# Performance work log

Hardware: AMD Instinct MI355X
Metric: run time of the kernel (lower is better)

The kernel has to match this reference:

```python
import jax, jax.numpy as jnp
import numpy as np


def setup_inputs() -> dict:
    key = jax.random.key(0)
    ks = jax.random.split(key, 6)
    B, T, D, H = 2, 2048, 1024, 16
    dk = D // H
    s = 0.02
    return {
        "x": jax.random.normal(ks[0], (B, T, D), dtype=jnp.float32),
        "Wq": jax.random.normal(ks[1], (H, dk, dk), dtype=jnp.float32) * s,
        "Wk": jax.random.normal(ks[2], (H, dk, dk), dtype=jnp.float32) * s,
        "Wv": jax.random.normal(ks[3], (H, dk, dk), dtype=jnp.float32) * s,
        "Wp": jax.random.normal(ks[4], (D, D), dtype=jnp.float32) * s,
        "bp": jnp.zeros((D,), dtype=jnp.float32),
    }


def reference(x, Wq, Wk, Wv, Wp, bp):
    B, T, D = x.shape
    H, dk, _ = Wq.shape
    # split into heads: [B, H, T, dk]
    xh = x.reshape(B, T, H, dk).transpose(0, 2, 1, 3)
    # per-head torch Linear (y = x @ W^T), all heads at once
    q = jnp.einsum('bhtd,hkd->bhtk', xh, Wq)
    k = jnp.einsum('bhtd,hkd->bhtk', xh, Wk)
    v = jnp.einsum('bhtd,hkd->bhtk', xh, Wv)
    scale = 1.0 / jnp.sqrt(jnp.float32(dk))  # original divides by sqrt(C) with C == d_k
    scores = jnp.einsum('bhqd,bhkd->bhqk', q, k) * scale
    causal = jnp.tril(jnp.ones((T, T), dtype=bool))
    scores = jnp.where(causal[None, None], scores, -jnp.inf)
    attn = jax.nn.softmax(scores, axis=-1)
    out = jnp.einsum('bhqk,bhkd->bhqd', attn, v)  # [B,H,T,dk]
    out = out.transpose(0, 2, 1, 3).reshape(B, T, D)  # concat heads
    return out @ Wp.T + bp
```

## Files before the change

kernel.cpp:

```cpp
#include <hip/hip_runtime.h>
#include <math.h>

#define B_ 2
#define T_ 2048
#define D_ 1024
#define H_ 16
#define DK 64
#define BH_ (B_*H_)

typedef __attribute__((ext_vector_type(8))) short short8;
typedef __attribute__((ext_vector_type(4))) float fragC;

#define MFMA32(A,B,C) __builtin_amdgcn_mfma_f32_16x16x32_bf16((A),(B),(C),0,0,0)

__device__ __forceinline__ unsigned short f2bf(float x) {
    union { float f; unsigned u; } c; c.f = x;
    unsigned r = c.u + 0x7fff + ((c.u >> 16) & 1);
    return (unsigned short)(r >> 16);
}

__device__ __forceinline__ unsigned pack2bf(float a, float b) {
    return (unsigned)f2bf(a) | ((unsigned)f2bf(b) << 16);
}

__device__ __forceinline__ unsigned permpack(float a, float b) {
    union { float f; unsigned u; } ca, cb; ca.f = a; cb.f = b;
    return __builtin_amdgcn_perm(cb.u, ca.u, 0x07060302);
}

__device__ __forceinline__ short8 packbf8(float4 a, float4 b) {
    union { short8 v; unsigned u[4]; } r;
    r.u[0] = pack2bf(a.x, a.y); r.u[1] = pack2bf(a.z, a.w);
    r.u[2] = pack2bf(b.x, b.y); r.u[3] = pack2bf(b.z, b.w);
    return r.v;
}

__device__ __forceinline__ void gload_lds16(const void* g, void* l) {
    __builtin_amdgcn_global_load_lds(
        (const __attribute__((address_space(1))) unsigned int*)g,
        (__attribute__((address_space(3))) unsigned int*)l, 16, 0, 0);
}

__global__ __launch_bounds__(256) void qkv_kernel(
    const float* __restrict__ x,
    const float* __restrict__ Wq, const float* __restrict__ Wk,
    const float* __restrict__ Wv, const float* __restrict__ Wp,
    unsigned short* __restrict__ Wb,
    unsigned short* __restrict__ q, unsigned short* __restrict__ k,
    unsigned short* __restrict__ vt)
{
    __shared__ unsigned short Wl[3*64*64];

    const int bh = blockIdx.x;
    const int b  = bh >> 4, h = bh & 15;
    const int t0 = blockIdx.y * 128;
    const int tid = threadIdx.x;
    const int wave = tid >> 6, lane = tid & 63;
    const int n = lane & 15, quad = lane >> 4;

    {
        const int L = bh + (blockIdx.y << 5);
        const float* src = Wp + (size_t)L*2048 + tid*8;
        float4 a = *(const float4*)src;
        float4 b2 = *(const float4*)(src + 4);
        *(uint4*)(Wb + (size_t)L*2048 + tid*8) =
            make_uint4(pack2bf(a.x, a.y), pack2bf(a.z, a.w),
                       pack2bf(b2.x, b2.y), pack2bf(b2.z, b2.w));
    }

    #pragma unroll
    for (int mat = 0; mat < 3; ++mat) {
        const float* ws = ((mat == 0) ? Wq : (mat == 1) ? Wk : Wv)
                          + (size_t)h * 4096;
        #pragma unroll
        for (int j = 0; j < 2; ++j) {
            const int e = (j*256 + tid) * 8;
            float4 a = *(const float4*)&ws[e];
            float4 b2 = *(const float4*)&ws[e + 4];
            *(uint4*)&Wl[mat*4096 + e] =
                make_uint4(pack2bf(a.x, a.y), pack2bf(a.z, a.w),
                           pack2bf(b2.x, b2.y), pack2bf(b2.z, b2.w));
        }
    }

    const int tw = t0 + wave*32;
    short8 xf[2][2];
    #pragma unroll
    for (int rt = 0; rt < 2; ++rt) {
        const float* xr = &x[((size_t)b*T_ + tw + rt*16 + n)*D_ + h*DK];
        float4 a0 = *(const float4*)&xr[quad*8];
        float4 a1 = *(const float4*)&xr[quad*8 + 4];
        xf[rt][0] = packbf8(a0, a1);
        float4 b0 = *(const float4*)&xr[32 + quad*8];
        float4 b1 = *(const float4*)&xr[32 + quad*8 + 4];
        xf[rt][1] = packbf8(b0, b1);
    }
    __syncthreads();

    const float qsc = 0.125f * 1.44269504088896340736f;
    const int tb0 = blockIdx.y*8 + wave*2;
    #pragma unroll
    for (int mat = 0; mat < 3; ++mat) {
        const int wbase = mat * 4096;
        #pragma unroll
        for (int ct = 0; ct < 4; ++ct) {
            short8 wf0 = *(const short8*)&Wl[wbase + (ct*16 + n)*64 + quad*8];
            short8 wf1 = *(const short8*)&Wl[wbase + (ct*16 + n)*64 + 32 + quad*8];
            if (mat < 2) {
                #pragma unroll
                for (int rt = 0; rt < 2; ++rt) {
                    fragC z = {0.f,0.f,0.f,0.f};
                    z = MFMA32(wf0, xf[rt][0], z);
                    z = MFMA32(wf1, xf[rt][1], z);
                    if (mat == 0) {
                        z[0] *= qsc; z[1] *= qsc; z[2] *= qsc; z[3] *= qsc;
                    }
                    unsigned short* dstg = (mat == 0) ? q : k;
                    unsigned short* dp = &dstg[((size_t)bh*128 + tb0 + rt)*1024
                                               + (ct*2 + (quad>>1))*128 + n*8 + (quad&1)*4];
                    *(uint2*)dp = make_uint2(pack2bf(z[0], z[1]), pack2bf(z[2], z[3]));
                }
            } else {
                uint4 pv4;
                {
                    fragC z = {0.f,0.f,0.f,0.f};
                    z = MFMA32(xf[0][0], wf0, z);
                    z = MFMA32(xf[0][1], wf1, z);
                    pv4.x = pack2bf(z[0], z[1]); pv4.y = pack2bf(z[2], z[3]);
                }
                {
                    fragC z = {0.f,0.f,0.f,0.f};
                    z = MFMA32(xf[1][0], wf0, z);
                    z = MFMA32(xf[1][1], wf1, z);
                    pv4.z = pack2bf(z[0], z[1]); pv4.w = pack2bf(z[2], z[3]);
                }
                const int ktv = tw >> 6, pv = (tw >> 5) & 1;
                unsigned short* dp = &vt[(size_t)bh*131072 + ktv*4096
                                         + ct*1024 + pv*512 + lane*8];
                *(uint4*)dp = pv4;
            }
        }
    }
}

__global__ __launch_bounds__(256, 2) void attn_kernel(
    const unsigned short* __restrict__ q, const unsigned short* __restrict__ k,
    const unsigned short* __restrict__ vt, unsigned short* __restrict__ aout)
{
    __shared__ fragC Os[4][4][4][64];
    __shared__ float Ls[4][4][16];

    const int id = blockIdx.x;
    const int xc = id & 7, p = id >> 3;
    const int jj = p & 3, s = p >> 2, g = s & 7, r = s >> 3;
    const int bh = xc*4 + jj;
    const int qt = (r == 0) ? 31 - g : (r == 1) ? g : (r == 2) ? 23 - g : 8 + g;

    const int b   = bh >> 4, h = bh & 15;
    const int tid = threadIdx.x;
    const int w = tid >> 6, lane = tid & 63;
    const int n = lane & 15, quad = lane >> 4;

    short8 qf[4][2];
    #pragma unroll
    for (int qc = 0; qc < 4; ++qc) {
        const unsigned short* qb = &q[((size_t)bh*128 + qt*4 + qc)*1024 + n*8];
        qf[qc][0] = *(const short8*)&qb[quad*128];
        qf[qc][1] = *(const short8*)&qb[(4 + quad)*128];
    }

    fragC o[4][4];
    #pragma unroll
    for (int qc = 0; qc < 4; ++qc)
        #pragma unroll
        for (int dt = 0; dt < 4; ++dt) o[qc][dt] = (fragC){0.f,0.f,0.f,0.f};
    fragC l[4];
    #pragma unroll
    for (int qc = 0; qc < 4; ++qc) l[qc] = (fragC){0.f,0.f,0.f,0.f};

    short8 ones8;
    #pragma unroll
    for (int jo = 0; jo < 8; ++jo) ones8[jo] = (short)0x3F80;

    const unsigned short* kg = &k[(size_t)bh*131072 + lane*8];
    const unsigned short* vg = &vt[(size_t)bh*131072 + lane*8];
    const int nt = qt + 1;

    short8 kf[4][2];
    short8 vv[4][2];

    int t = w;
    if (t < nt) {
        #pragma unroll
        for (int ct = 0; ct < 4; ++ct) {
            kf[ct][0] = *(const short8*)&kg[t*4096 + ct*1024];
            kf[ct][1] = *(const short8*)&kg[t*4096 + ct*1024 + 512];
        }
        #pragma unroll
        for (int dt = 0; dt < 4; ++dt) {
            vv[dt][0] = *(const short8*)&vg[t*4096 + dt*1024];
            vv[dt][1] = *(const short8*)&vg[t*4096 + dt*1024 + 512];
        }
    }

    for (; t < nt; t += 4) {
        const bool diag = (t == qt);
        unsigned pu[4][8];

        #pragma unroll
        for (int qp = 0; qp < 2; ++qp) {
            fragC c[2][4];
            __builtin_amdgcn_s_setprio(1);
            #pragma unroll
            for (int q2 = 0; q2 < 2; ++q2) {
                const int qc = qp*2 + q2;
                #pragma unroll
                for (int ct = 0; ct < 4; ++ct) {
                    fragC z = {0.f,0.f,0.f,0.f};
                    z = MFMA32(kf[ct][0], qf[qc][0], z);
                    z = MFMA32(kf[ct][1], qf[qc][1], z);
                    c[q2][ct] = z;
                }
            }
            __builtin_amdgcn_s_setprio(0);

            if (qp == 1 && t + 4 < nt) {
                #pragma unroll
                for (int ct = 0; ct < 4; ++ct) {
                    kf[ct][0] = *(const short8*)&kg[(t+4)*4096 + ct*1024];
                    kf[ct][1] = *(const short8*)&kg[(t+4)*4096 + ct*1024 + 512];
                }
            }

            #pragma unroll
            for (int q2 = 0; q2 < 2; ++q2) {
                const int qc = qp*2 + q2;
                #pragma unroll
                for (int ct = 0; ct < 4; ++ct) {
                    float p0 = exp2f(c[q2][ct][0]), p1 = exp2f(c[q2][ct][1]);
                    float p2 = exp2f(c[q2][ct][2]), p3 = exp2f(c[q2][ct][3]);
                    if (diag) {
                        const int lim = (qc*16 + n) - (ct*16 + quad*4);
                        if (0 > lim) p0 = 0.f;
                        if (1 > lim) p1 = 0.f;
                        if (2 > lim) p2 = 0.f;
                        if (3 > lim) p3 = 0.f;
                    }
                    pu[qc][(ct>>1)*4 + (ct&1)*2]     = permpack(p0, p1);
                    pu[qc][(ct>>1)*4 + (ct&1)*2 + 1] = permpack(p2, p3);
                }
            }
        }

        __builtin_amdgcn_s_setprio(1);
        #pragma unroll
        for (int qc = 0; qc < 4; ++qc) {
            #pragma unroll
            for (int pv = 0; pv < 2; ++pv) {
                union { unsigned u[4]; short8 v; } pk;
                pk.u[0] = pu[qc][pv*4];     pk.u[1] = pu[qc][pv*4 + 1];
                pk.u[2] = pu[qc][pv*4 + 2]; pk.u[3] = pu[qc][pv*4 + 3];
                l[qc] = MFMA32(ones8, pk.v, l[qc]);
                #pragma unroll
                for (int dt = 0; dt < 4; ++dt)
                    o[qc][dt] = MFMA32(vv[dt][pv], pk.v, o[qc][dt]);
            }
        }
        __builtin_amdgcn_s_setprio(0);

        if (t + 4 < nt) {
            #pragma unroll
            for (int dt = 0; dt < 4; ++dt) {
                vv[dt][0] = *(const short8*)&vg[(t+4)*4096 + dt*1024];
                vv[dt][1] = *(const short8*)&vg[(t+4)*4096 + dt*1024 + 512];
            }
        }
    }

    #pragma unroll
    for (int qc = 0; qc < 4; ++qc) {
        #pragma unroll
        for (int dt = 0; dt < 4; ++dt)
            Os[w][qc][dt][lane] = o[qc][dt];
        if (quad == 0) Ls[w][qc][n] = l[qc][0];
    }
    __syncthreads();

    const float lsum = Ls[0][w][n] + Ls[1][w][n] + Ls[2][w][n] + Ls[3][w][n];
    const float inv = 1.0f / lsum;
    const int q0 = qt*64 + w*16;
    unsigned short* dp = &aout[((size_t)b*T_ + q0 + n)*D_ + h*DK + quad*4];
    #pragma unroll
    for (int dt = 0; dt < 4; ++dt) {
        fragC sum = Os[0][w][dt][lane] + Os[1][w][dt][lane]
                  + Os[2][w][dt][lane] + Os[3][w][dt][lane];
        *(uint2*)(dp + dt*16) =
            make_uint2(pack2bf(sum[0]*inv, sum[1]*inv),
                       pack2bf(sum[2]*inv, sum[3]*inv));
    }
}

__global__ __launch_bounds__(256, 3) void proj_kernel(
    const unsigned short* __restrict__ A, const unsigned short* __restrict__ Wb,
    const float* __restrict__ bp, float* __restrict__ out)
{
    __shared__ unsigned short As[2][64*64];
    __shared__ unsigned short Bs[2][128*64];

    const int id = blockIdx.x;
    const int xcd = id & 7, idx = id >> 3;
    const int m0 = (xcd*8 + (idx & 7)) * 64;
    const int n0 = (idx >> 3) * 128;
    const int tid = threadIdx.x;
    const int wave = tid >> 6, lane = tid & 63;
    const int wm = wave & 1, wn = wave >> 1;
    const int n = lane & 15, quad = lane >> 4;

    const int arow = tid >> 3, acol = (tid & 7) * 8;
    const unsigned short* ag = &A [(size_t)(m0 + arow)*1024 + acol];
    const unsigned short* bg = &Wb[(size_t)(n0 + arow)*1024 + acol];

    fragC acc[2][4];
    #pragma unroll
    for (int i = 0; i < 2; ++i)
        #pragma unroll
        for (int j = 0; j < 4; ++j) acc[i][j] = (fragC){0.f,0.f,0.f,0.f};

    auto stage = [&](int bu, int kt) {
        #pragma unroll
        for (int i2 = 0; i2 < 2; ++i2)
            gload_lds16(ag + (size_t)i2*32*1024 + kt*64, &As[bu][i2*2048 + tid*8]);
        #pragma unroll
        for (int j2 = 0; j2 < 4; ++j2)
            gload_lds16(bg + (size_t)j2*32*1024 + kt*64, &Bs[bu][j2*2048 + tid*8]);
    };

    stage(0, 0);
    for (int kt = 0; kt < 16; ++kt) {
        __syncthreads();
        if (kt < 15) stage((kt + 1) & 1, kt + 1);
        const unsigned short* Ab = As[kt & 1];
        const unsigned short* Bb = Bs[kt & 1];
        #pragma unroll
        for (int kk = 0; kk < 2; ++kk) {
            short8 af[2], bf[4];
            #pragma unroll
            for (int i = 0; i < 2; ++i)
                af[i] = *(const short8*)&Ab[(wm*32 + i*16 + n)*64 + kk*32 + quad*8];
            #pragma unroll
            for (int j = 0; j < 4; ++j)
                bf[j] = *(const short8*)&Bb[(wn*64 + j*16 + n)*64 + kk*32 + quad*8];
            #pragma unroll
            for (int i = 0; i < 2; ++i)
                #pragma unroll
                for (int j = 0; j < 4; ++j)
                    acc[i][j] = MFMA32(af[i], bf[j], acc[i][j]);
        }
    }

    #pragma unroll
    for (int i = 0; i < 2; ++i) {
        #pragma unroll
        for (int r = 0; r < 4; ++r) {
            const int m = m0 + wm*32 + i*16 + quad*4 + r;
            #pragma unroll
            for (int j = 0; j < 4; ++j) {
                const int col = n0 + wn*64 + j*16 + n;
                out[(size_t)m*1024 + col] = acc[i][j][r] + bp[col];
            }
        }
    }
}

extern "C" void kernel_launch(void* const* d_in, const int* in_sizes, int n_in,
                              void* d_out, int out_size, void* d_ws, size_t ws_size,
                              hipStream_t stream)
{
    const float* x  = (const float*)d_in[0];
    const float* Wq = (const float*)d_in[1];
    const float* Wk = (const float*)d_in[2];
    const float* Wv = (const float*)d_in[3];
    const float* Wp = (const float*)d_in[4];
    const float* bp = (const float*)d_in[5];
    float* out = (float*)d_out;

    const size_t per = (size_t)BH_ * T_ * DK;
    unsigned short* qws   = (unsigned short*)d_ws;
    unsigned short* kws   = qws + per;
    unsigned short* vtws  = kws + per;
    unsigned short* aws   = vtws + per;
    unsigned short* wbws  = aws + per;

    qkv_kernel<<<dim3(BH_, T_/128), 256, 0, stream>>>(x, Wq, Wk, Wv, Wp, wbws,
                                                      qws, kws, vtws);
    attn_kernel<<<dim3(1024), 256, 0, stream>>>(qws, kws, vtws, aws);
    proj_kernel<<<dim3(512), 256, 0, stream>>>(aws, wbws, bp, out);
}
```

Baseline: 136.6 us.

## Replace ones-MFMA row sum with scalar accumulation and interleave QK/PV per chunk

The softmax denominator used to be computed with an extra MFMA against a vector of ones. It is now accumulated in scalar registers from bf16-truncated probabilities and reduced across quads with shuffles at the end. The score, exp and PV loop is restructured to handle one 16-row query chunk at a time, which drops the pu staging array and lowers register pressure. exp2f is swapped for the raw hardware builtin. Together these remove MFMA work and registers, in exchange for more VALU adds and slightly different rounding (truncation instead of round-to-nearest for P).

New measurement: 130.8 us (median of 2 runs). 4.3% less time.

```diff
diff --git a/kernel.cpp b/kernel.cpp
--- a/kernel.cpp
+++ b/kernel.cpp
@@ -13,6 +13,12 @@
 
 #define MFMA32(A,B,C) __builtin_amdgcn_mfma_f32_16x16x32_bf16((A),(B),(C),0,0,0)
 
+#if defined(__HIP_DEVICE_COMPILE__) && __has_builtin(__builtin_amdgcn_exp2f)
+#define EXP2 __builtin_amdgcn_exp2f
+#else
+#define EXP2 exp2f
+#endif
+
 __device__ __forceinline__ unsigned short f2bf(float x) {
     union { float f; unsigned u; } c; c.f = x;
     unsigned r = c.u + 0x7fff + ((c.u >> 16) & 1);
@@ -26,6 +32,12 @@
 __device__ __forceinline__ unsigned permpack(float a, float b) {
     union { float f; unsigned u; } ca, cb; ca.f = a; cb.f = b;
     return __builtin_amdgcn_perm(cb.u, ca.u, 0x07060302);
+}
+
+__device__ __forceinline__ float truncbf(float x) {
+    union { float f; unsigned u; } c; c.f = x;
+    c.u &= 0xffff0000u;
+    return c.f;
 }
 
 __device__ __forceinline__ short8 packbf8(float4 a, float4 b) {
@@ -174,13 +186,7 @@
     for (int qc = 0; qc < 4; ++qc)
         #pragma unroll
         for (int dt = 0; dt < 4; ++dt) o[qc][dt] = (fragC){0.f,0.f,0.f,0.f};
-    fragC l[4];
-    #pragma unroll
-    for (int qc = 0; qc < 4; ++qc) l[qc] = (fragC){0.f,0.f,0.f,0.f};
-
-    short8 ones8;
-    #pragma unroll
-    for (int jo = 0; jo < 8; ++jo) ones8[jo] = (short)0x3F80;
+    float lsc[4] = {0.f, 0.f, 0.f, 0.f};
 
     const unsigned short* kg = &k[(size_t)bh*131072 + lane*8];
     const unsigned short* vg = &vt[(size_t)bh*131072 + lane*8];
@@ -205,26 +211,20 @@
 
     for (; t < nt; t += 4) {
         const bool diag = (t == qt);
-        unsigned pu[4][8];
-
-        #pragma unroll
-        for (int qp = 0; qp < 2; ++qp) {
-            fragC c[2][4];
+        #pragma unroll
+        for (int qc = 0; qc < 4; ++qc) {
+            fragC c[4];
             __builtin_amdgcn_s_setprio(1);
             #pragma unroll
-            for (int q2 = 0; q2 < 2; ++q2) {
-                const int qc = qp*2 + q2;
-                #pragma unroll
-                for (int ct = 0; ct < 4; ++ct) {
-                    fragC z = {0.f,0.f,0.f,0.f};
-                    z = MFMA32(kf[ct][0], qf[qc][0], z);
-                    z = MFMA32(kf[ct][1], qf[qc][1], z);
-                    c[q2][ct] = z;
-                }
+            for (int ct = 0; ct < 4; ++ct) {
+                fragC z = {0.f,0.f,0.f,0.f};
+                z = MFMA32(kf[ct][0], qf[qc][0], z);
+                z = MFMA32(kf[ct][1], qf[qc][1], z);
+                c[ct] = z;
             }
             __builtin_amdgcn_s_setprio(0);
 
-            if (qp == 1 && t + 4 < nt) {
+            if (qc == 3 && t + 4 < nt) {
                 #pragma unroll
                 for (int ct = 0; ct < 4; ++ct) {
                     kf[ct][0] = *(const short8*)&kg[(t+4)*4096 + ct*1024];
@@ -232,41 +232,36 @@
                 }
             }
 
-            #pragma unroll
-            for (int q2 = 0; q2 < 2; ++q2) {
-                const int qc = qp*2 + q2;
-                #pragma unroll
-                for (int ct = 0; ct < 4; ++ct) {
-                    float p0 = exp2f(c[q2][ct][0]), p1 = exp2f(c[q2][ct][1]);
-                    float p2 = exp2f(c[q2][ct][2]), p3 = exp2f(c[q2][ct][3]);
-                    if (diag) {
-                        const int lim = (qc*16 + n) - (ct*16 + quad*4);
-                        if (0 > lim) p0 = 0.f;
-                        if (1 > lim) p1 = 0.f;
-                        if (2 > lim) p2 = 0.f;
-                        if (3 > lim) p3 = 0.f;
-                    }
-                    pu[qc][(ct>>1)*4 + (ct&1)*2]     = permpack(p0, p1);
-                    pu[qc][(ct>>1)*4 + (ct&1)*2 + 1] = permpack(p2, p3);
-                }
-            }
-        }
-
-        __builtin_amdgcn_s_setprio(1);
-        #pragma unroll
-        for (int qc = 0; qc < 4; ++qc) {
+            union { unsigned u[4]; short8 v; } pb[2];
+            float ls = 0.f;
+            #pragma unroll
+            for (int ct = 0; ct < 4; ++ct) {
+                float p0 = EXP2(c[ct][0]), p1 = EXP2(c[ct][1]);
+                float p2 = EXP2(c[ct][2]), p3 = EXP2(c[ct][3]);
+                if (diag) {
+                    const int lim = (qc*16 + n) - (ct*16 + quad*4);
+                    if (0 > lim) p0 = 0.f;
+                    if (1 > lim) p1 = 0.f;
+                    if (2 > lim) p2 = 0.f;
+                    if (3 > lim) p3 = 0.f;
+                }
+                p0 = truncbf(p0); p1 = truncbf(p1);
+                p2 = truncbf(p2); p3 = truncbf(p3);
+                ls += (p0 + p1) + (p2 + p3);
+                pb[ct >> 1].u[(ct & 1)*2]     = permpack(p0, p1);
+                pb[ct >> 1].u[(ct & 1)*2 + 1] = permpack(p2, p3);
+            }
+            lsc[qc] += ls;
+
+            __builtin_amdgcn_s_setprio(1);
             #pragma unroll
             for (int pv = 0; pv < 2; ++pv) {
-                union { unsigned u[4]; short8 v; } pk;
-                pk.u[0] = pu[qc][pv*4];     pk.u[1] = pu[qc][pv*4 + 1];
-                pk.u[2] = pu[qc][pv*4 + 2]; pk.u[3] = pu[qc][pv*4 + 3];
-                l[qc] = MFMA32(ones8, pk.v, l[qc]);
                 #pragma unroll
                 for (int dt = 0; dt < 4; ++dt)
-                    o[qc][dt] = MFMA32(vv[dt][pv], pk.v, o[qc][dt]);
-            }
-        }
-        __builtin_amdgcn_s_setprio(0);
+                    o[qc][dt] = MFMA32(vv[dt][pv], pb[pv].v, o[qc][dt]);
+            }
+            __builtin_amdgcn_s_setprio(0);
+        }
 
         if (t + 4 < nt) {
             #pragma unroll
@@ -279,10 +274,16 @@
 
     #pragma unroll
     for (int qc = 0; qc < 4; ++qc) {
+        lsc[qc] += __shfl_xor(lsc[qc], 16);
+        lsc[qc] += __shfl_xor(lsc[qc], 32);
+    }
+
+    #pragma unroll
+    for (int qc = 0; qc < 4; ++qc) {
         #pragma unroll
         for (int dt = 0; dt < 4; ++dt)
             Os[w][qc][dt][lane] = o[qc][dt];
-        if (quad == 0) Ls[w][qc][n] = l[qc][0];
+        if (quad == 0) Ls[w][qc][n] = lsc[qc];
     }
     __syncthreads();
 
```
